# Optimization experiments

Measured on AMD Instinct MI355X. Metric: run time of the kernel, lower is better.

The kernel has to match this reference:

```python
import jax, jax.numpy as jnp
import numpy as np
import math

WS = 8          # window_size
H = 16          # num_heads
C = 512         # dim
D = C // H      # head dim


def _relative_coords_table():
    # (2*WS-1, 2*WS-1, 2), Swin-V2 log-spaced continuous coords
    r = jnp.arange(-(WS - 1), WS, dtype=jnp.float32)
    t = jnp.stack(jnp.meshgrid(r, r, indexing='ij'), axis=-1)
    t = t / (WS - 1) * 8.0
    return jnp.sign(t) * jnp.log2(jnp.abs(t) + 1.0) / np.float32(np.log2(8.0))


def _relative_position_index():
    # (WS*WS, WS*WS) int32 indices into the (2*WS-1)^2 bias table
    coords = np.stack(np.meshgrid(np.arange(WS), np.arange(WS), indexing='ij'))  # (2,WS,WS)
    cf = coords.reshape(2, -1)                                # (2, N)
    rel = cf[:, :, None] - cf[:, None, :]                     # (2, N, N)
    rel = rel.transpose(1, 2, 0)                              # (N, N, 2)
    rel[:, :, 0] += WS - 1
    rel[:, :, 1] += WS - 1
    rel[:, :, 0] *= 2 * WS - 1
    return jnp.asarray(rel.sum(-1), dtype=jnp.int32)


def setup_inputs() -> dict:
    key = jax.random.key(0)
    ks = jax.random.split(key, 9)
    B, N = 2048, WS * WS
    s = 0.02
    return {
        'hidden_states': jax.random.normal(ks[0], (B, N, C), jnp.float32),
        'q_w': jax.random.normal(ks[1], (C, C), jnp.float32) * s,
        'q_b': jnp.zeros((C,), jnp.float32),
        'k_w': jax.random.normal(ks[2], (C, C), jnp.float32) * s,
        'v_w': jax.random.normal(ks[3], (C, C), jnp.float32) * s,
        'v_b': jnp.zeros((C,), jnp.float32),
        'logit_scale': jnp.full((H, 1, 1), np.float32(math.log(10.0))),
        'cpb_w1': jax.random.normal(ks[4], (512, 2), jnp.float32) * s,
        'cpb_b1': jnp.zeros((512,), jnp.float32),
        'cpb_w2': jax.random.normal(ks[5], (H, 512), jnp.float32) * s,
    }


def reference(hidden_states, q_w, q_b, k_w, v_w, v_b, logit_scale,
              cpb_w1, cpb_b1, cpb_w2):
    B, N, _ = hidden_states.shape

    def heads(x):  # (B,N,C) -> (B,H,N,D)
        return x.reshape(B, N, H, D).transpose(0, 2, 1, 3)

    q = heads(hidden_states @ q_w.T + q_b)
    k = heads(hidden_states @ k_w.T)
    v = heads(hidden_states @ v_w.T + v_b)

    # cosine-similarity attention with clamped learnable logit scale
    qn = q / jnp.linalg.norm(q, axis=-1, keepdims=True)
    kn = k / jnp.linalg.norm(k, axis=-1, keepdims=True)
    scale = jnp.exp(jnp.minimum(logit_scale, np.float32(math.log(100.0))))  # (H,1,1)
    scores = jnp.einsum('bhnd,bhmd->bhnm', qn, kn) * scale

    # continuous relative position bias MLP + gather + sigmoid scale
    table = _relative_coords_table().reshape(-1, 2)            # (225, 2)
    hbias = jax.nn.relu(table @ cpb_w1.T + cpb_b1) @ cpb_w2.T  # (225, H)
    idx = _relative_position_index().reshape(-1)               # (N*N,)
    rpb = hbias[idx].reshape(N, N, H).transpose(2, 0, 1)       # (H, N, N)
    scores = scores + 16.0 * jax.nn.sigmoid(rpb)[None]

    probs = jax.nn.softmax(scores, axis=-1)
    ctx = jnp.einsum('bhnm,bhmd->bhnd', probs, v)
    return ctx.transpose(0, 2, 1, 3).reshape(B, N, C)
```

## Files before the change

### kernel.cpp

```cpp
#include <hip/hip_runtime.h>
#include <hip/hip_bf16.h>
#include <cstdint>
#include <cstddef>

typedef __attribute__((ext_vector_type(4))) float f32x4;
typedef __attribute__((ext_vector_type(8))) short short8;
typedef unsigned short ushort_t;

__device__ __forceinline__ ushort_t f2bf(float f) {
  unsigned u = __builtin_bit_cast(unsigned, f);
  u = u + 0x7FFFu + ((u >> 16) & 1u);
  return (ushort_t)(u >> 16);
}
__device__ __forceinline__ void load_lds16(const void* g, void* l) {
  __builtin_amdgcn_global_load_lds((const __attribute__((address_space(1))) void*)g,
                                   (__attribute__((address_space(3))) void*)l, 16, 0, 0);
}

__device__ __forceinline__ int swzA(int row, int b) { return row*128 + (b ^ ((row & 7) << 4)); }
__device__ __forceinline__ int swzQ(int row, int b) { return row*64  + (b ^ (((row >> 1) & 3) << 4)); }
__device__ __forceinline__ int swzV(int d,   int b) { return d*256   + (b ^ ((d & 7) << 4)); }

__global__ __launch_bounds__(256) void k_cvt_bf16(const float4* __restrict__ in,
                                                  ushort_t* __restrict__ outp, int n4) {
  int i = blockIdx.x * 256 + threadIdx.x;
  int stride = gridDim.x * 256;
  for (; i < n4; i += stride) {
    float4 v = in[i];
    ushort4 o = { f2bf(v.x), f2bf(v.y), f2bf(v.z), f2bf(v.w) };
    *(ushort4*)(outp + (size_t)i * 4) = o;
  }
}

__global__ __launch_bounds__(256) void k_wcat(const float* __restrict__ qw, const float* __restrict__ qb,
                                              const float* __restrict__ kw, const float* __restrict__ vw,
                                              const float* __restrict__ vb,
                                              ushort_t* __restrict__ Wcat, float* __restrict__ bcat) {
  int o = blockIdx.x;
  int h = o / 96, r = o % 96;
  const float* src; float bias;
  if (r < 32)      { src = qw + (size_t)(h*32 + r)      * 512; bias = qb[h*32 + r]; }
  else if (r < 64) { src = kw + (size_t)(h*32 + r - 32) * 512; bias = 0.f; }
  else             { src = vw + (size_t)(h*32 + r - 64) * 512; bias = vb[h*32 + r - 64]; }
  int t = threadIdx.x;
  Wcat[(size_t)o*512 + t]       = f2bf(src[t]);
  Wcat[(size_t)o*512 + t + 256] = f2bf(src[t + 256]);
  if (t == 0) bcat[o] = bias;
}

__global__ __launch_bounds__(256) void k_bias(const float* __restrict__ w1, const float* __restrict__ b1,
                                              const float* __restrict__ w2, float* __restrict__ bias16) {
  int t = blockIdx.x;
  int a = t / 15, b = t % 15;
  float x = (float)(a - 7) * (8.f / 7.f);
  float y = (float)(b - 7) * (8.f / 7.f);
  float fx = (x == 0.f) ? 0.f : copysignf(log2f(fabsf(x) + 1.f) * (1.f / 3.f), x);
  float fy = (y == 0.f) ? 0.f : copysignf(log2f(fabsf(y) + 1.f) * (1.f / 3.f), y);
  int wv = threadIdx.x >> 6, lane = threadIdx.x & 63;
  float acc[4] = {0.f, 0.f, 0.f, 0.f};
  for (int it = 0; it < 8; ++it) {
    int j = it*64 + lane;
    float act = fmaxf(fx * w1[2*j] + fy * w1[2*j + 1] + b1[j], 0.f);
#pragma unroll
    for (int hh = 0; hh < 4; ++hh)
      acc[hh] += act * w2[(wv*4 + hh)*512 + j];
  }
#pragma unroll
  for (int hh = 0; hh < 4; ++hh) {
    float v = acc[hh];
    for (int s = 1; s < 64; s <<= 1) v += __shfl_xor(v, s);
    if (lane == 0) bias16[t*16 + wv*4 + hh] = 16.f / (1.f + __expf(-v));
  }
}

#define BS_OFF 16384
#define KS_OFF 8192
#define VT_OFF 16384
#define PS_OFF 24576

__global__ __launch_bounds__(256) void k_main(const ushort_t* __restrict__ hbf,
                                              const ushort_t* __restrict__ Wcat,
                                              const float* __restrict__ bcat,
                                              const float* __restrict__ bias16,
                                              const float* __restrict__ lscale,
                                              float* __restrict__ out) {
  __shared__ __align__(128) char lb_raw[32768];
  char* lb = lb_raw;

  int bid = blockIdx.x;
  int wg = (bid & 7) * 2048 + (bid >> 3);
  int mtile = wg >> 4;
  int h     = wg & 15;

  int tid = threadIdx.x;
  int w = tid >> 6, lane = tid & 63;
  int lm = lane & 15, lg = lane >> 4;

  const ushort_t* Ag = hbf  + (size_t)mtile * 128 * 512;
  const ushort_t* Wg = Wcat + (size_t)h * 96 * 512;

  int rA0 = w*32      + (lane >> 2);
  int rA1 = w*32 + 16 + (lane >> 2);
  int rB0 = w*16      + (lane >> 2);
  int rB1 = 64 + w*16 + (lane >> 2);
  int sl  = lane & 3;
  int offA0 = rA0*512 + (sl ^ ((rA0 >> 1) & 3))*8;
  int offA1 = rA1*512 + (sl ^ ((rA1 >> 1) & 3))*8;
  int offB0 = rB0*512 + (sl ^ ((rB0 >> 1) & 3))*8;
  int offB1 = rB1*512 + (sl ^ ((rB1 >> 1) & 3))*8;

  f32x4 acc[2][6] = {};

#define STAGE(ksn, bsel) do {                                                  \
    int kk0 = (ksn) * 32;                                                      \
    load_lds16(Ag + offA0 + kk0, lb + (bsel)*8192 + (w*2+0)*1024);             \
    load_lds16(Ag + offA1 + kk0, lb + (bsel)*8192 + (w*2+1)*1024);             \
    load_lds16(Wg + offB0 + kk0, lb + BS_OFF + (bsel)*6144 + w*1024);          \
    if (w < 2)                                                                 \
      load_lds16(Wg + offB1 + kk0, lb + BS_OFF + (bsel)*6144 + (4+w)*1024);    \
  } while (0)

  STAGE(0, 0);
#pragma unroll
  for (int ks = 0; ks < 16; ++ks) {
    int cur = ks & 1;
    if (ks < 15) {
      STAGE(ks + 1, cur ^ 1);
      if (w < 2) asm volatile("s_waitcnt vmcnt(4)" ::: "memory");
      else       asm volatile("s_waitcnt vmcnt(3)" ::: "memory");
    } else {
      asm volatile("s_waitcnt vmcnt(0)" ::: "memory");
    }
    asm volatile("s_barrier" ::: "memory");

    const char* Ab = lb + cur*8192;
    const char* Bb = lb + BS_OFF + cur*6144;
    short8 av0 = *(const short8*)(Ab + swzQ(w*32      + lm, lg*16));
    short8 av1 = *(const short8*)(Ab + swzQ(w*32 + 16 + lm, lg*16));
    short8 bv[6];
#pragma unroll
    for (int j = 0; j < 6; ++j)
      bv[j] = *(const short8*)(Bb + swzQ(j*16 + lm, lg*16));
#pragma unroll
    for (int j = 0; j < 6; ++j)
      acc[0][j] = __builtin_amdgcn_mfma_f32_16x16x32_bf16(av0, bv[j], acc[0][j], 0, 0, 0);
#pragma unroll
    for (int j = 0; j < 6; ++j)
      acc[1][j] = __builtin_amdgcn_mfma_f32_16x16x32_bf16(av1, bv[j], acc[1][j], 0, 0, 0);

    asm volatile("s_barrier" ::: "memory");
  }
#undef STAGE

  __builtin_amdgcn_s_setprio(1);
  float scl = __expf(fminf(lscale[h], 4.6051701860f));
  float bb[6];
#pragma unroll
  for (int nj = 0; nj < 6; ++nj) bb[nj] = bcat[h*96 + nj*16 + lm];

#pragma unroll
  for (int i = 0; i < 2; ++i) {
#pragma unroll
    for (int r = 0; r < 4; ++r) {
      float q0 = acc[i][0][r] + bb[0], q1 = acc[i][1][r] + bb[1];
      float k0 = acc[i][2][r],         k1 = acc[i][3][r];
      float ssq = q0*q0 + q1*q1;
      float ssk = k0*k0 + k1*k1;
      ssq += __shfl_xor(ssq, 1); ssq += __shfl_xor(ssq, 2);
      ssq += __shfl_xor(ssq, 4); ssq += __shfl_xor(ssq, 8);
      ssk += __shfl_xor(ssk, 1); ssk += __shfl_xor(ssk, 2);
      ssk += __shfl_xor(ssk, 4); ssk += __shfl_xor(ssk, 8);
      float rq = rsqrtf(ssq) * scl;
      float rk = rsqrtf(ssk);
      int row = w*32 + i*16 + lg*4 + r;
      *(ushort_t*)(lb + swzQ(row, lm*2))                  = f2bf(q0 * rq);
      *(ushort_t*)(lb + swzQ(row, 32 + lm*2))             = f2bf(q1 * rq);
      *(ushort_t*)(lb + KS_OFF + swzQ(row, lm*2))         = f2bf(k0 * rk);
      *(ushort_t*)(lb + KS_OFF + swzQ(row, 32 + lm*2))    = f2bf(k1 * rk);
    }
#pragma unroll
    for (int j = 0; j < 2; ++j) {
      ushort4 pk;
      pk.x = f2bf(acc[i][4+j][0] + bb[4+j]);
      pk.y = f2bf(acc[i][4+j][1] + bb[4+j]);
      pk.z = f2bf(acc[i][4+j][2] + bb[4+j]);
      pk.w = f2bf(acc[i][4+j][3] + bb[4+j]);
      int d = j*16 + lm, tokb = (w*32 + i*16 + lg*4) * 2;
      *(ushort4*)(lb + VT_OFF + swzV(d, tokb)) = pk;
    }
  }
  __syncthreads();

  float bfrag[4][4];
#pragma unroll
  for (int ci = 0; ci < 4; ++ci) {
    int m = ci*16 + lm, rm = m >> 3, cm = m & 7;
#pragma unroll
    for (int r = 0; r < 4; ++r) {
      int n = w*16 + lg*4 + r;
      int idx = ((n >> 3) - rm + 7)*15 + ((n & 7) - cm + 7);
      bfrag[ci][r] = bias16[idx*16 + h];
    }
  }

#pragma unroll
  for (int win = 0; win < 2; ++win) {
    short8 aq = *(const short8*)(lb + swzQ(win*64 + w*16 + lm, lg*16));
    f32x4 p[4];
#pragma unroll
    for (int ci = 0; ci < 4; ++ci) {
      short8 bk = *(const short8*)(lb + KS_OFF + swzQ(win*64 + ci*16 + lm, lg*16));
      f32x4 z = {0.f, 0.f, 0.f, 0.f};
      f32x4 s = __builtin_amdgcn_mfma_f32_16x16x32_bf16(aq, bk, z, 0, 0, 0);
#pragma unroll
      for (int r = 0; r < 4; ++r)
        p[ci][r] = __expf(s[r] + bfrag[ci][r]);
    }
#pragma unroll
    for (int ci = 0; ci < 4; ++ci)
#pragma unroll
      for (int r = 0; r < 4; ++r) {
        int row = w*16 + lg*4 + r;
        *(ushort_t*)(lb + PS_OFF + swzA(row, (ci*16 + lm)*2)) = f2bf(p[ci][r]);
      }
    float rs[4];
#pragma unroll
    for (int r = 0; r < 4; ++r) {
      float s = p[0][r] + p[1][r] + p[2][r] + p[3][r];
      s += __shfl_xor(s, 1); s += __shfl_xor(s, 2);
      s += __shfl_xor(s, 4); s += __shfl_xor(s, 8);
      rs[r] = 1.f / s;
    }
    f32x4 oacc[2] = {};
#pragma unroll
    for (int kk = 0; kk < 2; ++kk) {
      short8 ap = *(const short8*)(lb + PS_OFF + swzA(w*16 + lm, kk*64 + lg*16));
#pragma unroll
      for (int ci = 0; ci < 2; ++ci) {
        short8 bvv = *(const short8*)(lb + VT_OFF + swzV(ci*16 + lm, win*128 + kk*64 + lg*16));
        oacc[ci] = __builtin_amdgcn_mfma_f32_16x16x32_bf16(ap, bvv, oacc[ci], 0, 0, 0);
      }
    }
    size_t gw = (size_t)mtile*2 + win;
#pragma unroll
    for (int ci = 0; ci < 2; ++ci)
#pragma unroll
      for (int r = 0; r < 4; ++r) {
        int n = w*16 + lg*4 + r;
        out[(gw*64 + n)*512 + h*32 + ci*16 + lm] = oacc[ci][r] * rs[r];
      }
  }
  __builtin_amdgcn_s_setprio(0);
}

extern "C" void kernel_launch(void* const* d_in, const int* in_sizes, int n_in,
                              void* d_out, int out_size, void* d_ws, size_t ws_size,
                              hipStream_t stream) {
  (void)in_sizes; (void)n_in; (void)out_size; (void)ws_size;
  const float* hidden = (const float*)d_in[0];
  const float* q_w    = (const float*)d_in[1];
  const float* q_b    = (const float*)d_in[2];
  const float* k_w    = (const float*)d_in[3];
  const float* v_w    = (const float*)d_in[4];
  const float* v_b    = (const float*)d_in[5];
  const float* lscale = (const float*)d_in[6];
  const float* cpb_w1 = (const float*)d_in[7];
  const float* cpb_b1 = (const float*)d_in[8];
  const float* cpb_w2 = (const float*)d_in[9];
  float* out = (float*)d_out;

  char* wsb = (char*)d_ws;
  ushort_t* hbf    = (ushort_t*)wsb;
  ushort_t* Wcat   = (ushort_t*)(wsb + 134217728);
  float*    bcat   = (float*)(wsb + 135790592);
  float*    bias16 = (float*)(wsb + 135796736);

  hipLaunchKernelGGL(k_cvt_bf16, dim3(2048), dim3(256), 0, stream,
                     (const float4*)hidden, hbf, 16777216);
  hipLaunchKernelGGL(k_wcat, dim3(1536), dim3(256), 0, stream,
                     q_w, q_b, k_w, v_w, v_b, Wcat, bcat);
  hipLaunchKernelGGL(k_bias, dim3(225), dim3(256), 0, stream,
                     cpb_w1, cpb_b1, cpb_w2, bias16);
  hipLaunchKernelGGL(k_main, dim3(16384), dim3(256), 0, stream,
                     hbf, Wcat, bcat, bias16, lscale, out);
}
```

Measured before the change: 472.3 us.

## Double M-tile to 256 rows per block with 512 threads, reuse weight tile

Each workgroup now covers 256 token rows (four windows) for one head using 8 waves, so each staged weight tile is shared by twice as many rows and the grid is halved. The attention phase is reorganised so each wave handles 32 query rows of one window, with per-wave P slots in LDS and bias values loaded inline instead of precomputed in registers. LDS per block grows to 48 KB and launch bounds request 6 waves per SIMD, which may limit occupancy and raise register pressure.

```diff
diff --git a/kernel.cpp b/kernel.cpp
--- a/kernel.cpp
+++ b/kernel.cpp
@@ -17,9 +17,8 @@
                                    (__attribute__((address_space(3))) void*)l, 16, 0, 0);
 }
 
-__device__ __forceinline__ int swzA(int row, int b) { return row*128 + (b ^ ((row & 7) << 4)); }
 __device__ __forceinline__ int swzQ(int row, int b) { return row*64  + (b ^ (((row >> 1) & 3) << 4)); }
-__device__ __forceinline__ int swzV(int d,   int b) { return d*256   + (b ^ ((d & 7) << 4)); }
+__device__ __forceinline__ int swzV5(int d,  int b) { return d*512   + (b ^ ((d & 7) << 4)); }
 
 __global__ __launch_bounds__(256) void k_cvt_bf16(const float4* __restrict__ in,
                                                   ushort_t* __restrict__ outp, int n4) {
@@ -73,22 +72,22 @@
   }
 }
 
-#define BS_OFF 16384
-#define KS_OFF 8192
-#define VT_OFF 16384
-#define PS_OFF 24576
-
-__global__ __launch_bounds__(256) void k_main(const ushort_t* __restrict__ hbf,
-                                              const ushort_t* __restrict__ Wcat,
-                                              const float* __restrict__ bcat,
-                                              const float* __restrict__ bias16,
-                                              const float* __restrict__ lscale,
-                                              float* __restrict__ out) {
-  __shared__ __align__(128) char lb_raw[32768];
+#define ABUF(bsel) ((bsel)*16384)
+#define BBUF(bsel) (32768 + (bsel)*6144)
+#define KS_OFF 16384
+#define VT_OFF 32768
+
+__global__ __launch_bounds__(512, 6) void k_main(const ushort_t* __restrict__ hbf,
+                                                 const ushort_t* __restrict__ Wcat,
+                                                 const float* __restrict__ bcat,
+                                                 const float* __restrict__ bias16,
+                                                 const float* __restrict__ lscale,
+                                                 float* __restrict__ out) {
+  __shared__ __align__(128) char lb_raw[49152];
   char* lb = lb_raw;
 
   int bid = blockIdx.x;
-  int wg = (bid & 7) * 2048 + (bid >> 3);
+  int wg = (bid & 7) * 1024 + (bid >> 3);
   int mtile = wg >> 4;
   int h     = wg & 15;
 
@@ -96,28 +95,22 @@
   int w = tid >> 6, lane = tid & 63;
   int lm = lane & 15, lg = lane >> 4;
 
-  const ushort_t* Ag = hbf  + (size_t)mtile * 128 * 512;
+  const ushort_t* Ag = hbf  + (size_t)mtile * 256 * 512;
   const ushort_t* Wg = Wcat + (size_t)h * 96 * 512;
 
-  int rA0 = w*32      + (lane >> 2);
-  int rA1 = w*32 + 16 + (lane >> 2);
-  int rB0 = w*16      + (lane >> 2);
-  int rB1 = 64 + w*16 + (lane >> 2);
-  int sl  = lane & 3;
+  int rA0 = tid >> 2, rA1 = 128 + (tid >> 2);
+  int sl  = tid & 3;
   int offA0 = rA0*512 + (sl ^ ((rA0 >> 1) & 3))*8;
   int offA1 = rA1*512 + (sl ^ ((rA1 >> 1) & 3))*8;
-  int offB0 = rB0*512 + (sl ^ ((rB0 >> 1) & 3))*8;
-  int offB1 = rB1*512 + (sl ^ ((rB1 >> 1) & 3))*8;
 
   f32x4 acc[2][6] = {};
 
 #define STAGE(ksn, bsel) do {                                                  \
     int kk0 = (ksn) * 32;                                                      \
-    load_lds16(Ag + offA0 + kk0, lb + (bsel)*8192 + (w*2+0)*1024);             \
-    load_lds16(Ag + offA1 + kk0, lb + (bsel)*8192 + (w*2+1)*1024);             \
-    load_lds16(Wg + offB0 + kk0, lb + BS_OFF + (bsel)*6144 + w*1024);          \
-    if (w < 2)                                                                 \
-      load_lds16(Wg + offB1 + kk0, lb + BS_OFF + (bsel)*6144 + (4+w)*1024);    \
+    load_lds16(Ag + offA0 + kk0, lb + ABUF(bsel) + tid*16);                    \
+    load_lds16(Ag + offA1 + kk0, lb + ABUF(bsel) + 8192 + tid*16);             \
+    if (tid < 384)                                                             \
+      load_lds16(Wg + offA0 + kk0, lb + BBUF(bsel) + tid*16);                  \
   } while (0)
 
   STAGE(0, 0);
@@ -126,15 +119,15 @@
     int cur = ks & 1;
     if (ks < 15) {
       STAGE(ks + 1, cur ^ 1);
-      if (w < 2) asm volatile("s_waitcnt vmcnt(4)" ::: "memory");
-      else       asm volatile("s_waitcnt vmcnt(3)" ::: "memory");
+      if (tid < 384) asm volatile("s_waitcnt vmcnt(3)" ::: "memory");
+      else           asm volatile("s_waitcnt vmcnt(2)" ::: "memory");
     } else {
       asm volatile("s_waitcnt vmcnt(0)" ::: "memory");
     }
     asm volatile("s_barrier" ::: "memory");
 
-    const char* Ab = lb + cur*8192;
-    const char* Bb = lb + BS_OFF + cur*6144;
+    const char* Ab = lb + ABUF(cur);
+    const char* Bb = lb + BBUF(cur);
     short8 av0 = *(const short8*)(Ab + swzQ(w*32      + lm, lg*16));
     short8 av1 = *(const short8*)(Ab + swzQ(w*32 + 16 + lm, lg*16));
     short8 bv[6];
@@ -173,10 +166,10 @@
       float rq = rsqrtf(ssq) * scl;
       float rk = rsqrtf(ssk);
       int row = w*32 + i*16 + lg*4 + r;
-      *(ushort_t*)(lb + swzQ(row, lm*2))                  = f2bf(q0 * rq);
-      *(ushort_t*)(lb + swzQ(row, 32 + lm*2))             = f2bf(q1 * rq);
-      *(ushort_t*)(lb + KS_OFF + swzQ(row, lm*2))         = f2bf(k0 * rk);
-      *(ushort_t*)(lb + KS_OFF + swzQ(row, 32 + lm*2))    = f2bf(k1 * rk);
+      *(ushort_t*)(lb + swzQ(row, lm*2))               = f2bf(q0 * rq);
+      *(ushort_t*)(lb + swzQ(row, 32 + lm*2))          = f2bf(q1 * rq);
+      *(ushort_t*)(lb + KS_OFF + swzQ(row, lm*2))      = f2bf(k0 * rk);
+      *(ushort_t*)(lb + KS_OFF + swzQ(row, 32 + lm*2)) = f2bf(k1 * rk);
     }
 #pragma unroll
     for (int j = 0; j < 2; ++j) {
@@ -186,69 +179,67 @@
       pk.z = f2bf(acc[i][4+j][2] + bb[4+j]);
       pk.w = f2bf(acc[i][4+j][3] + bb[4+j]);
       int d = j*16 + lm, tokb = (w*32 + i*16 + lg*4) * 2;
-      *(ushort4*)(lb + VT_OFF + swzV(d, tokb)) = pk;
+      *(ushort4*)(lb + VT_OFF + swzV5(d, tokb)) = pk;
     }
   }
   __syncthreads();
 
-  float bfrag[4][4];
-#pragma unroll
-  for (int ci = 0; ci < 4; ++ci) {
-    int m = ci*16 + lm, rm = m >> 3, cm = m & 7;
-#pragma unroll
-    for (int r = 0; r < 4; ++r) {
-      int n = w*16 + lg*4 + r;
-      int idx = ((n >> 3) - rm + 7)*15 + ((n & 7) - cm + 7);
-      bfrag[ci][r] = bias16[idx*16 + h];
-    }
-  }
-
-#pragma unroll
-  for (int win = 0; win < 2; ++win) {
-    short8 aq = *(const short8*)(lb + swzQ(win*64 + w*16 + lm, lg*16));
-    f32x4 p[4];
+  int win = w >> 1;
+  int nb  = (w & 1) * 32;
+#pragma unroll
+  for (int mi = 0; mi < 2; ++mi) {
+    short8 aq = *(const short8*)(lb + swzQ(w*32 + mi*16 + lm, lg*16));
+    f32x4 s4[4];
 #pragma unroll
     for (int ci = 0; ci < 4; ++ci) {
       short8 bk = *(const short8*)(lb + KS_OFF + swzQ(win*64 + ci*16 + lm, lg*16));
       f32x4 z = {0.f, 0.f, 0.f, 0.f};
-      f32x4 s = __builtin_amdgcn_mfma_f32_16x16x32_bf16(aq, bk, z, 0, 0, 0);
-#pragma unroll
-      for (int r = 0; r < 4; ++r)
-        p[ci][r] = __expf(s[r] + bfrag[ci][r]);
-    }
-#pragma unroll
-    for (int ci = 0; ci < 4; ++ci)
+      s4[ci] = __builtin_amdgcn_mfma_f32_16x16x32_bf16(aq, bk, z, 0, 0, 0);
+    }
+#pragma unroll
+    for (int ci = 0; ci < 4; ++ci) {
+      int m = ci*16 + lm, rm = m >> 3, cm = m & 7;
 #pragma unroll
       for (int r = 0; r < 4; ++r) {
-        int row = w*16 + lg*4 + r;
-        *(ushort_t*)(lb + PS_OFF + swzA(row, (ci*16 + lm)*2)) = f2bf(p[ci][r]);
+        int n = nb + mi*16 + lg*4 + r;
+        int idx = ((n >> 3) - rm + 7)*15 + ((n & 7) - cm + 7);
+        s4[ci][r] = __expf(s4[ci][r] + bias16[idx*16 + h]);
       }
+    }
     float rs[4];
 #pragma unroll
     for (int r = 0; r < 4; ++r) {
-      float s = p[0][r] + p[1][r] + p[2][r] + p[3][r];
+      float s = s4[0][r] + s4[1][r] + s4[2][r] + s4[3][r];
       s += __shfl_xor(s, 1); s += __shfl_xor(s, 2);
       s += __shfl_xor(s, 4); s += __shfl_xor(s, 8);
       rs[r] = 1.f / s;
     }
+    char* slot = lb + w*2048 + mi*1024;
     f32x4 oacc[2] = {};
 #pragma unroll
     for (int kk = 0; kk < 2; ++kk) {
-      short8 ap = *(const short8*)(lb + PS_OFF + swzA(w*16 + lm, kk*64 + lg*16));
-#pragma unroll
-      for (int ci = 0; ci < 2; ++ci) {
-        short8 bvv = *(const short8*)(lb + VT_OFF + swzV(ci*16 + lm, win*128 + kk*64 + lg*16));
-        oacc[ci] = __builtin_amdgcn_mfma_f32_16x16x32_bf16(ap, bvv, oacc[ci], 0, 0, 0);
+#pragma unroll
+      for (int cc = 0; cc < 2; ++cc) {
+        int ci = kk*2 + cc;
+#pragma unroll
+        for (int r = 0; r < 4; ++r) {
+          int pr = lg*4 + r;
+          *(ushort_t*)(slot + swzQ(pr, cc*32 + lm*2)) = f2bf(s4[ci][r]);
+        }
       }
-    }
-    size_t gw = (size_t)mtile*2 + win;
-#pragma unroll
-    for (int ci = 0; ci < 2; ++ci)
-#pragma unroll
-      for (int r = 0; r < 4; ++r) {
-        int n = w*16 + lg*4 + r;
-        out[(gw*64 + n)*512 + h*32 + ci*16 + lm] = oacc[ci][r] * rs[r];
+      short8 ap = *(const short8*)(slot + swzQ(lm, lg*16));
+#pragma unroll
+      for (int c2 = 0; c2 < 2; ++c2) {
+        short8 bvv = *(const short8*)(lb + VT_OFF + swzV5(c2*16 + lm, win*128 + kk*64 + lg*16));
+        oacc[c2] = __builtin_amdgcn_mfma_f32_16x16x32_bf16(ap, bvv, oacc[c2], 0, 0, 0);
       }
+    }
+    size_t rowb = (size_t)mtile*256 + w*32 + mi*16;
+#pragma unroll
+    for (int c2 = 0; c2 < 2; ++c2)
+#pragma unroll
+      for (int r = 0; r < 4; ++r)
+        out[(rowb + lg*4 + r)*512 + h*32 + c2*16 + lm] = oacc[c2][r] * rs[r];
   }
   __builtin_amdgcn_s_setprio(0);
 }
@@ -281,6 +272,6 @@
                      q_w, q_b, k_w, v_w, v_b, Wcat, bcat);
   hipLaunchKernelGGL(k_bias, dim3(225), dim3(256), 0, stream,
                      cpb_w1, cpb_b1, cpb_w2, bias16);
-  hipLaunchKernelGGL(k_main, dim3(16384), dim3(256), 0, stream,
+  hipLaunchKernelGGL(k_main, dim3(8192), dim3(512), 0, stream,
                      hbf, Wcat, bcat, bias16, lscale, out);
 }
```

Result: slower. 773.7 us (+63.8%).
